# Kernel optimization log

Hardware: AMD Instinct MI355X
Metric: run time of the kernel (lower is better)

The kernel has to match this reference:

```python
import jax, jax.numpy as jnp
import numpy as np

B = 65536  # batch size

def setup_inputs() -> dict:
    key = jax.random.key(0)
    ks = jax.random.split(key, 6)
    x = jax.random.normal(ks[0], (B, 784), dtype=jnp.float32)
    conv_w = jax.random.normal(ks[1], (3, 3), dtype=jnp.float32) * 0.1
    in_size = (28 - 3 + 1) * (28 - 3 + 1)  # 676
    w1 = jax.random.normal(ks[2], (in_size, 300), dtype=jnp.float32) * 0.05
    b1 = jax.random.normal(ks[3], (300,), dtype=jnp.float32) * 0.05
    w2 = jax.random.normal(ks[4], (300, 10), dtype=jnp.float32) * 0.05
    b2 = jax.random.normal(ks[5], (10,), dtype=jnp.float32) * 0.05
    return {"x": x, "conv_w": conv_w, "w1": w1, "b1": b1, "w2": w2, "b2": b2}

def _convolve(img, conv_w):
    # img: [B,28,28]; conv_w: [kh,kw]. Valid cross-correlation (tensordot of each
    # window with the un-flipped kernel), matching the original Convolve().
    out = jax.lax.conv_general_dilated(
        img[:, None, :, :],            # [B,1,28,28]  NCHW
        conv_w[None, None, :, :],      # [1,1,3,3]    OIHW (no flip -> cross-correlation)
        window_strides=(1, 1),
        padding="VALID",
        dimension_numbers=("NCHW", "OIHW", "NCHW"),
    )
    return out[:, 0]  # [B,26,26]

def reference(x, conv_w, w1, b1, w2, b2):
    b = x.shape[0]
    img = x.reshape(b, 28, 28)
    feat = _convolve(img, conv_w).reshape(b, -1)      # [B,676]
    h1 = jax.nn.relu(feat @ w1 + b1)                  # [B,300]
    return h1 @ w2 + b2                               # [B,10]
```

## Files before the change

### kernel.cpp

```cpp
#include <hip/hip_runtime.h>
#include <hip/hip_bf16.h>

typedef __attribute__((ext_vector_type(8))) short bf16x8;
typedef __attribute__((ext_vector_type(4))) float f32x4;
typedef __attribute__((ext_vector_type(4))) unsigned int u32x4;
typedef unsigned short u16;
typedef unsigned int u32;

static constexpr int KDIM  = 784;
static constexpr int KP    = 800;
static constexpr int NDIM  = 300;
static constexpr int NP    = 320;
static constexpr int DDIM  = 10;
static constexpr int BM    = 256;
static constexpr int BK    = 32;
static constexpr int NSTEP = 25;
static constexpr int H1STR = 328;
static constexpr int NROW  = 65536;
static constexpr int NTHR  = 512;
static constexpr int ABYTES = 32768;
static constexpr int BBYTES = 20480;
static constexpr int BBASE  = 98304;

__device__ __forceinline__ u16 f2bf(float f) {
  unsigned u = __builtin_bit_cast(unsigned, f);
  u += 0x7fffu + ((u >> 16) & 1u);
  return (u16)(u >> 16);
}
__device__ __forceinline__ u32 pk2(float a, float b) {
  u32 r;
  asm("v_cvt_pk_bf16_f32 %0, %1, %2" : "=v"(r) : "v"(a), "v"(b));
  return r;
}
__device__ __forceinline__ void gll16(const void* g, void* l) {
  __builtin_amdgcn_global_load_lds(
      (const __attribute__((address_space(1))) void*)g,
      (__attribute__((address_space(3))) void*)l, 16, 0, 0);
}

__global__ void build_weff(const float* __restrict__ cw,
                           const float* __restrict__ w1,
                           u16* __restrict__ weff) {
  int idx = blockIdx.x * 256 + threadIdx.x;
  if (idx >= NP * KP) return;
  int n = idx / KP;
  int k = idx - n * KP;
  float acc = 0.f;
  if (n < NDIM && k < KDIM) {
    int r = k / 28, c = k - (k / 28) * 28;
    #pragma unroll
    for (int dr = 0; dr < 3; ++dr) {
      int orr = r - dr;
      if ((unsigned)orr < 26u) {
        #pragma unroll
        for (int dc = 0; dc < 3; ++dc) {
          int oc = c - dc;
          if ((unsigned)oc < 26u)
            acc += cw[dr * 3 + dc] * w1[(orr * 26 + oc) * NDIM + n];
        }
      }
    }
  }
  weff[n * KP + k] = f2bf(acc);
}

__global__ void __launch_bounds__(NTHR, 2)
fused_mlp(const float* __restrict__ x, const float* __restrict__ b1,
          const float* __restrict__ w2, const float* __restrict__ b2,
          const u16* __restrict__ weff, float* __restrict__ out) {
  __shared__ __align__(16) u16 lds[69632];

  const int tid  = threadIdx.x;
  const int wv   = tid >> 6;
  const int lane = tid & 63;
  const int l16  = lane & 15;
  const int lhi  = lane >> 4;
  const int wm   = wv >> 2;
  const int wn   = wv & 3;
  const int bm   = blockIdx.x * BM;
  const int wvn  = wn * 80;

  int aRow[4], aQg[4];
  #pragma unroll
  for (int it = 0; it < 4; ++it) {
    int s = tid + it * NTHR;
    aRow[it] = s >> 3;
    aQg[it]  = (s & 7) ^ (aRow[it] & 7);
  }
  int bRow[3], bQg[3];
  #pragma unroll
  for (int i = 0; i < 3; ++i) {
    int s = (i < 2) ? (tid + i * NTHR) : (1024 + (tid & 255));
    bRow[i] = s >> 2;
    bQg[i]  = (s & 3) ^ (bRow[i] & 3);
  }

  auto stageA = [&](int bufi, int t) {
    char* base = (char*)lds + bufi * ABYTES;
    int k0 = (t < NSTEP) ? t * BK : 0;
    #pragma unroll
    for (int it = 0; it < 4; ++it) {
      int kof = k0 + aQg[it] * 4;
      if (kof >= KDIM) kof = aQg[it] * 4;
      gll16(x + (size_t)(bm + aRow[it]) * KDIM + kof,
            base + (tid + it * NTHR) * 16);
    }
  };
  auto stageB = [&](int bufi, int t) {
    char* base = (char*)lds + BBASE + bufi * BBYTES;
    int k0 = (t < NSTEP) ? t * BK : 0;
    #pragma unroll
    for (int i = 0; i < 3; ++i) {
      int s = (i < 2) ? (tid + i * NTHR) : (1024 + (tid & 255));
      gll16(weff + (size_t)bRow[i] * KP + k0 + bQg[i] * 8, base + s * 16);
    }
  };

  f32x4 acc[8][5];
  #pragma unroll
  for (int mi = 0; mi < 8; ++mi)
    #pragma unroll
    for (int ni = 0; ni < 5; ++ni)
      acc[mi][ni] = (f32x4){0.f, 0.f, 0.f, 0.f};

  auto compute = [&](int abufi, int bbufi) {
    const f32x4* Af = (const f32x4*)((char*)lds + abufi * ABYTES);
    const u16*   Bb = (const u16*)((char*)lds + BBASE + bbufi * BBYTES);
    bf16x8 bfr[5];
    #pragma unroll
    for (int ni = 0; ni < 5; ++ni) {
      int n = wvn + ni * 16 + l16;
      int slot = n * 4 + (lhi ^ (n & 3));
      bfr[ni] = *reinterpret_cast<const bf16x8*>(Bb + slot * 8);
    }
    #pragma unroll
    for (int mi = 0; mi < 8; ++mi) {
      int R = wm * 128 + mi * 16 + l16;
      f32x4 a0 = Af[R * 8 + ((2 * lhi)     ^ (R & 7))];
      f32x4 a1 = Af[R * 8 + ((2 * lhi + 1) ^ (R & 7))];
      u32x4 amu = { pk2(a0[0], a0[1]), pk2(a0[2], a0[3]),
                    pk2(a1[0], a1[1]), pk2(a1[2], a1[3]) };
      bf16x8 am = __builtin_bit_cast(bf16x8, amu);
      #pragma unroll
      for (int ni = 0; ni < 5; ++ni)
        acc[mi][ni] = __builtin_amdgcn_mfma_f32_16x16x32_bf16(am, bfr[ni], acc[mi][ni], 0, 0, 0);
    }
  };

  stageA(0, 0);
  stageB(0, 0);
  stageA(1, 1);
  asm volatile("s_waitcnt vmcnt(4)" ::: "memory");
  __builtin_amdgcn_s_barrier();
  __builtin_amdgcn_sched_barrier(0);

  for (int t = 0; t < NSTEP; ++t) {
    stageB((t + 1) & 1, t + 1);
    stageA((t + 2) % 3, t + 2);
    __builtin_amdgcn_sched_barrier(0);
    compute(t % 3, t & 1);
    __builtin_amdgcn_sched_barrier(0);
    asm volatile("s_waitcnt vmcnt(4)" ::: "memory");
    __builtin_amdgcn_s_barrier();
    __builtin_amdgcn_sched_barrier(0);
  }
  __syncthreads();

  u16* H1  = lds;
  u16* W2T = lds + 20992;

  for (int i = tid; i < 16 * NP; i += NTHR) {
    int d = i / NP, n = i - (i / NP) * NP;
    float v = (d < DDIM && n < NDIM) ? w2[n * DDIM + d] : 0.f;
    W2T[d * H1STR + n] = f2bf(v);
  }
  float biasv[5];
  #pragma unroll
  for (int ni = 0; ni < 5; ++ni) {
    int col = wvn + ni * 16 + l16;
    biasv[ni] = (col < NDIM) ? b1[col] : 0.f;
  }

  #pragma unroll
  for (int p = 0; p < 4; ++p) {
    if (wm == (p >> 1)) {
      #pragma unroll
      for (int mj = 0; mj < 4; ++mj) {
        int mi = (p & 1) * 4 + mj;
        #pragma unroll
        for (int ni = 0; ni < 5; ++ni) {
          int col = wvn + ni * 16 + l16;
          int rb  = mj * 16 + lhi * 4;
          #pragma unroll
          for (int r = 0; r < 4; ++r) {
            float h = acc[mi][ni][r] + biasv[ni];
            H1[(rb + r) * H1STR + col] = f2bf(fmaxf(h, 0.f));
          }
        }
      }
    }
    __syncthreads();
    if (wv < 4) {
      f32x4 a2c = (f32x4){0.f, 0.f, 0.f, 0.f};
      #pragma unroll
      for (int ks = 0; ks < NP / 32; ++ks) {
        bf16x8 a2 = *reinterpret_cast<const bf16x8*>(
            H1 + (wv * 16 + l16) * H1STR + ks * 32 + lhi * 8);
        bf16x8 bw = *reinterpret_cast<const bf16x8*>(
            W2T + l16 * H1STR + ks * 32 + lhi * 8);
        a2c = __builtin_amdgcn_mfma_f32_16x16x32_bf16(a2, bw, a2c, 0, 0, 0);
      }
      if (l16 < DDIM) {
        float bb = b2[l16];
        #pragma unroll
        for (int r = 0; r < 4; ++r) {
          int row = bm + p * 64 + wv * 16 + lhi * 4 + r;
          out[(size_t)row * DDIM + l16] = a2c[r] + bb;
        }
      }
    }
    __syncthreads();
  }
}

extern "C" void kernel_launch(void* const* d_in, const int* in_sizes, int n_in,
                              void* d_out, int out_size, void* d_ws, size_t ws_size,
                              hipStream_t stream) {
  const float* x  = (const float*)d_in[0];
  const float* cw = (const float*)d_in[1];
  const float* w1 = (const float*)d_in[2];
  const float* b1 = (const float*)d_in[3];
  const float* w2 = (const float*)d_in[4];
  const float* b2 = (const float*)d_in[5];
  float* out = (float*)d_out;
  u16* weff = (u16*)d_ws;

  hipLaunchKernelGGL(build_weff, dim3((NP * KP + 255) / 256), dim3(256), 0, stream,
                     cw, w1, weff);
  hipLaunchKernelGGL(fused_mlp, dim3(NROW / BM), dim3(NTHR), 0, stream,
                     x, b1, w2, b2, weff, out);
}
```

Measured before the change: 61.70 us.

## Halve row tile to 128 and simplify to double-buffered pipeline

Shrinks the per-block row tile from 256 to 128, which halves the accumulator registers and the A staging buffers. LDS use drops from about 136KB to 72KB and the grid doubles to 512 blocks. The triple-buffered A pipeline with fine-grained vmcnt waits is replaced by simple double buffering with a full __syncthreads each step. The goal is better occupancy and load balance across CUs. In exchange, each B (weff) tile is reloaded by twice as many blocks, and the coarser sync gives less overlap of loads with compute.

```diff
diff --git a/kernel.cpp b/kernel.cpp
--- a/kernel.cpp
+++ b/kernel.cpp
@@ -12,15 +12,15 @@
 static constexpr int NDIM  = 300;
 static constexpr int NP    = 320;
 static constexpr int DDIM  = 10;
-static constexpr int BM    = 256;
+static constexpr int BM    = 128;
 static constexpr int BK    = 32;
 static constexpr int NSTEP = 25;
 static constexpr int H1STR = 328;
 static constexpr int NROW  = 65536;
 static constexpr int NTHR  = 512;
-static constexpr int ABYTES = 32768;
+static constexpr int ABYTES = 16384;
 static constexpr int BBYTES = 20480;
-static constexpr int BBASE  = 98304;
+static constexpr int BBASE  = 32768;
 
 __device__ __forceinline__ u16 f2bf(float f) {
   unsigned u = __builtin_bit_cast(unsigned, f);
@@ -68,7 +68,7 @@
 fused_mlp(const float* __restrict__ x, const float* __restrict__ b1,
           const float* __restrict__ w2, const float* __restrict__ b2,
           const u16* __restrict__ weff, float* __restrict__ out) {
-  __shared__ __align__(16) u16 lds[69632];
+  __shared__ __align__(16) u16 lds[36864];
 
   const int tid  = threadIdx.x;
   const int wv   = tid >> 6;
@@ -80,26 +80,27 @@
   const int bm   = blockIdx.x * BM;
   const int wvn  = wn * 80;
 
-  int aRow[4], aQg[4];
-  #pragma unroll
-  for (int it = 0; it < 4; ++it) {
+  int aRow[2], aQg[2];
+  #pragma unroll
+  for (int it = 0; it < 2; ++it) {
     int s = tid + it * NTHR;
     aRow[it] = s >> 3;
     aQg[it]  = (s & 7) ^ (aRow[it] & 7);
   }
-  int bRow[3], bQg[3];
+  int bRow[3], bQg[3], bSlot[3];
   #pragma unroll
   for (int i = 0; i < 3; ++i) {
     int s = (i < 2) ? (tid + i * NTHR) : (1024 + (tid & 255));
-    bRow[i] = s >> 2;
-    bQg[i]  = (s & 3) ^ (bRow[i] & 3);
+    bSlot[i] = s;
+    bRow[i]  = s >> 2;
+    bQg[i]   = (s & 3) ^ (bRow[i] & 3);
   }
 
   auto stageA = [&](int bufi, int t) {
     char* base = (char*)lds + bufi * ABYTES;
-    int k0 = (t < NSTEP) ? t * BK : 0;
-    #pragma unroll
-    for (int it = 0; it < 4; ++it) {
+    int k0 = t * BK;
+    #pragma unroll
+    for (int it = 0; it < 2; ++it) {
       int kof = k0 + aQg[it] * 4;
       if (kof >= KDIM) kof = aQg[it] * 4;
       gll16(x + (size_t)(bm + aRow[it]) * KDIM + kof,
@@ -108,24 +109,22 @@
   };
   auto stageB = [&](int bufi, int t) {
     char* base = (char*)lds + BBASE + bufi * BBYTES;
-    int k0 = (t < NSTEP) ? t * BK : 0;
-    #pragma unroll
-    for (int i = 0; i < 3; ++i) {
-      int s = (i < 2) ? (tid + i * NTHR) : (1024 + (tid & 255));
-      gll16(weff + (size_t)bRow[i] * KP + k0 + bQg[i] * 8, base + s * 16);
-    }
+    int k0 = t * BK;
+    #pragma unroll
+    for (int i = 0; i < 3; ++i)
+      gll16(weff + (size_t)bRow[i] * KP + k0 + bQg[i] * 8, base + bSlot[i] * 16);
   };
 
-  f32x4 acc[8][5];
-  #pragma unroll
-  for (int mi = 0; mi < 8; ++mi)
+  f32x4 acc[4][5];
+  #pragma unroll
+  for (int mi = 0; mi < 4; ++mi)
     #pragma unroll
     for (int ni = 0; ni < 5; ++ni)
       acc[mi][ni] = (f32x4){0.f, 0.f, 0.f, 0.f};
 
-  auto compute = [&](int abufi, int bbufi) {
-    const f32x4* Af = (const f32x4*)((char*)lds + abufi * ABYTES);
-    const u16*   Bb = (const u16*)((char*)lds + BBASE + bbufi * BBYTES);
+  auto compute = [&](int bufi) {
+    const f32x4* Af = (const f32x4*)((char*)lds + bufi * ABYTES);
+    const u16*   Bb = (const u16*)((char*)lds + BBASE + bufi * BBYTES);
     bf16x8 bfr[5];
     #pragma unroll
     for (int ni = 0; ni < 5; ++ni) {
@@ -134,8 +133,8 @@
       bfr[ni] = *reinterpret_cast<const bf16x8*>(Bb + slot * 8);
     }
     #pragma unroll
-    for (int mi = 0; mi < 8; ++mi) {
-      int R = wm * 128 + mi * 16 + l16;
+    for (int mi = 0; mi < 4; ++mi) {
+      int R = wm * 64 + mi * 16 + l16;
       f32x4 a0 = Af[R * 8 + ((2 * lhi)     ^ (R & 7))];
       f32x4 a1 = Af[R * 8 + ((2 * lhi + 1) ^ (R & 7))];
       u32x4 amu = { pk2(a0[0], a0[1]), pk2(a0[2], a0[3]),
@@ -149,22 +148,16 @@
 
   stageA(0, 0);
   stageB(0, 0);
-  stageA(1, 1);
-  asm volatile("s_waitcnt vmcnt(4)" ::: "memory");
-  __builtin_amdgcn_s_barrier();
-  __builtin_amdgcn_sched_barrier(0);
+  __syncthreads();
 
   for (int t = 0; t < NSTEP; ++t) {
-    stageB((t + 1) & 1, t + 1);
-    stageA((t + 2) % 3, t + 2);
-    __builtin_amdgcn_sched_barrier(0);
-    compute(t % 3, t & 1);
-    __builtin_amdgcn_sched_barrier(0);
-    asm volatile("s_waitcnt vmcnt(4)" ::: "memory");
-    __builtin_amdgcn_s_barrier();
-    __builtin_amdgcn_sched_barrier(0);
-  }
-  __syncthreads();
+    if (t + 1 < NSTEP) {
+      stageB((t + 1) & 1, t + 1);
+      stageA((t + 1) & 1, t + 1);
+    }
+    compute(t & 1);
+    __syncthreads();
+  }
 
   u16* H1  = lds;
   u16* W2T = lds + 20992;
@@ -182,15 +175,14 @@
   }
 
   #pragma unroll
-  for (int p = 0; p < 4; ++p) {
-    if (wm == (p >> 1)) {
+  for (int p = 0; p < 2; ++p) {
+    if (wm == p) {
       #pragma unroll
-      for (int mj = 0; mj < 4; ++mj) {
-        int mi = (p & 1) * 4 + mj;
+      for (int mi = 0; mi < 4; ++mi) {
         #pragma unroll
         for (int ni = 0; ni < 5; ++ni) {
           int col = wvn + ni * 16 + l16;
-          int rb  = mj * 16 + lhi * 4;
+          int rb  = mi * 16 + lhi * 4;
           #pragma unroll
           for (int r = 0; r < 4; ++r) {
             float h = acc[mi][ni][r] + biasv[ni];
```

Result: slower. 87.81 us (+42.3%).

## Load weight fragments directly from global and deepen A pipeline to four stages

Applied to the files above, without the earlier changes.

Drops LDS staging of the effective weight matrix and has each wave load its bf16 B fragments straight from global memory (L2-resident) into registers every K step. The freed LDS is used for a fourth x buffer, so the A prefetch runs three steps ahead. The goal is to remove B staging traffic and LDS reads, and to hide x load latency better. In exchange, the direct global B loads in the critical path add latency and redundant L2 traffic across waves. The vmcnt waits were changed to match the new per-thread load count.

```diff
diff --git a/kernel.cpp b/kernel.cpp
--- a/kernel.cpp
+++ b/kernel.cpp
@@ -19,8 +19,6 @@
 static constexpr int NROW  = 65536;
 static constexpr int NTHR  = 512;
 static constexpr int ABYTES = 32768;
-static constexpr int BBYTES = 20480;
-static constexpr int BBASE  = 98304;
 
 __device__ __forceinline__ u16 f2bf(float f) {
   unsigned u = __builtin_bit_cast(unsigned, f);
@@ -68,7 +66,7 @@
 fused_mlp(const float* __restrict__ x, const float* __restrict__ b1,
           const float* __restrict__ w2, const float* __restrict__ b2,
           const u16* __restrict__ weff, float* __restrict__ out) {
-  __shared__ __align__(16) u16 lds[69632];
+  __shared__ __align__(16) u16 lds[65536];
 
   const int tid  = threadIdx.x;
   const int wv   = tid >> 6;
@@ -87,13 +85,6 @@
     aRow[it] = s >> 3;
     aQg[it]  = (s & 7) ^ (aRow[it] & 7);
   }
-  int bRow[3], bQg[3];
-  #pragma unroll
-  for (int i = 0; i < 3; ++i) {
-    int s = (i < 2) ? (tid + i * NTHR) : (1024 + (tid & 255));
-    bRow[i] = s >> 2;
-    bQg[i]  = (s & 3) ^ (bRow[i] & 3);
-  }
 
   auto stageA = [&](int bufi, int t) {
     char* base = (char*)lds + bufi * ABYTES;
@@ -106,15 +97,11 @@
             base + (tid + it * NTHR) * 16);
     }
   };
-  auto stageB = [&](int bufi, int t) {
-    char* base = (char*)lds + BBASE + bufi * BBYTES;
-    int k0 = (t < NSTEP) ? t * BK : 0;
-    #pragma unroll
-    for (int i = 0; i < 3; ++i) {
-      int s = (i < 2) ? (tid + i * NTHR) : (1024 + (tid & 255));
-      gll16(weff + (size_t)bRow[i] * KP + k0 + bQg[i] * 8, base + s * 16);
-    }
-  };
+
+  int bOff[5];
+  #pragma unroll
+  for (int ni = 0; ni < 5; ++ni)
+    bOff[ni] = (wvn + ni * 16 + l16) * KP + lhi * 8;
 
   f32x4 acc[8][5];
   #pragma unroll
@@ -123,16 +110,23 @@
     for (int ni = 0; ni < 5; ++ni)
       acc[mi][ni] = (f32x4){0.f, 0.f, 0.f, 0.f};
 
-  auto compute = [&](int abufi, int bbufi) {
-    const f32x4* Af = (const f32x4*)((char*)lds + abufi * ABYTES);
-    const u16*   Bb = (const u16*)((char*)lds + BBASE + bbufi * BBYTES);
+  stageA(0, 0);
+  stageA(1, 1);
+  stageA(2, 2);
+  asm volatile("s_waitcnt vmcnt(8)" ::: "memory");
+  __builtin_amdgcn_s_barrier();
+  __builtin_amdgcn_sched_barrier(0);
+
+  for (int t = 0; t < NSTEP; ++t) {
     bf16x8 bfr[5];
     #pragma unroll
-    for (int ni = 0; ni < 5; ++ni) {
-      int n = wvn + ni * 16 + l16;
-      int slot = n * 4 + (lhi ^ (n & 3));
-      bfr[ni] = *reinterpret_cast<const bf16x8*>(Bb + slot * 8);
-    }
+    for (int ni = 0; ni < 5; ++ni)
+      bfr[ni] = *reinterpret_cast<const bf16x8*>(weff + bOff[ni] + t * BK);
+    __builtin_amdgcn_sched_barrier(0);
+    stageA((t + 3) & 3, t + 3);
+    __builtin_amdgcn_sched_barrier(0);
+
+    const f32x4* Af = (const f32x4*)((char*)lds + (t & 3) * ABYTES);
     #pragma unroll
     for (int mi = 0; mi < 8; ++mi) {
       int R = wm * 128 + mi * 16 + l16;
@@ -145,20 +139,6 @@
       for (int ni = 0; ni < 5; ++ni)
         acc[mi][ni] = __builtin_amdgcn_mfma_f32_16x16x32_bf16(am, bfr[ni], acc[mi][ni], 0, 0, 0);
     }
-  };
-
-  stageA(0, 0);
-  stageB(0, 0);
-  stageA(1, 1);
-  asm volatile("s_waitcnt vmcnt(4)" ::: "memory");
-  __builtin_amdgcn_s_barrier();
-  __builtin_amdgcn_sched_barrier(0);
-
-  for (int t = 0; t < NSTEP; ++t) {
-    stageB((t + 1) & 1, t + 1);
-    stageA((t + 2) % 3, t + 2);
-    __builtin_amdgcn_sched_barrier(0);
-    compute(t % 3, t & 1);
     __builtin_amdgcn_sched_barrier(0);
     asm volatile("s_waitcnt vmcnt(4)" ::: "memory");
     __builtin_amdgcn_s_barrier();
```

New measurement: 77.64 us. 1.26x slower.

## Stage w1 rows in LDS for weff build and halve epilogue passes

Applied to the files above, without the earlier changes.

Rewrites build_weff to run one block per input image row. Each block stages the three contributing w1 rows in shared memory, computes the folded weights, and writes them out through an LDS transpose so the global stores are coalesced instead of strided reads from global memory. The fused kernel's epilogue now stores 128 rows of H1 per pass and uses all 8 waves for the second GEMM, so it runs 2 passes instead of 4 and needs fewer barriers. The trade-off is that build_weff launches only 28 blocks, which leaves most CUs idle and adds some LDS reindexing work.

```diff
diff --git a/kernel.cpp b/kernel.cpp
--- a/kernel.cpp
+++ b/kernel.cpp
@@ -19,8 +19,8 @@
 static constexpr int NROW  = 65536;
 static constexpr int NTHR  = 512;
 static constexpr int ABYTES = 32768;
-static constexpr int BBYTES = 20480;
-static constexpr int BBASE  = 98304;
+static constexpr int BBASEU = 49152;
+static constexpr int BU     = 10240;
 
 __device__ __forceinline__ u16 f2bf(float f) {
   unsigned u = __builtin_bit_cast(unsigned, f);
@@ -38,30 +38,56 @@
       (__attribute__((address_space(3))) void*)l, 16, 0, 0);
 }
 
-__global__ void build_weff(const float* __restrict__ cw,
-                           const float* __restrict__ w1,
-                           u16* __restrict__ weff) {
-  int idx = blockIdx.x * 256 + threadIdx.x;
-  if (idx >= NP * KP) return;
-  int n = idx / KP;
-  int k = idx - n * KP;
-  float acc = 0.f;
-  if (n < NDIM && k < KDIM) {
-    int r = k / 28, c = k - (k / 28) * 28;
-    #pragma unroll
-    for (int dr = 0; dr < 3; ++dr) {
-      int orr = r - dr;
-      if ((unsigned)orr < 26u) {
-        #pragma unroll
-        for (int dc = 0; dc < 3; ++dc) {
-          int oc = c - dc;
-          if ((unsigned)oc < 26u)
-            acc += cw[dr * 3 + dc] * w1[(orr * 26 + oc) * NDIM + n];
+__global__ void __launch_bounds__(256)
+build_weff(const float* __restrict__ cw, const float* __restrict__ w1,
+           u16* __restrict__ weff) {
+  __shared__ float w1s[78 * 300];
+  __shared__ u16 outT[NP * 28];
+
+  const int r   = blockIdx.x;
+  const int tid = threadIdx.x;
+
+  for (int i = tid; i < 3 * 7800; i += 256) {
+    int j = i / 7800, rem = i - j * 7800;
+    int orr = r - 2 + j;
+    w1s[i] = ((unsigned)orr < 26u) ? w1[orr * 7800 + rem] : 0.f;
+  }
+  float c9[9];
+  #pragma unroll
+  for (int q = 0; q < 9; ++q) c9[q] = cw[q];
+  __syncthreads();
+
+  for (int i = tid; i < NP * 28; i += 256) {
+    int n = i / 28, c = i - (i / 28) * 28;
+    float acc = 0.f;
+    if (n < NDIM) {
+      #pragma unroll
+      for (int dr = 0; dr < 3; ++dr) {
+        int orr = r - dr;
+        if ((unsigned)orr < 26u) {
+          #pragma unroll
+          for (int dc = 0; dc < 3; ++dc) {
+            int oc = c - dc;
+            if ((unsigned)oc < 26u)
+              acc += c9[dr * 3 + dc] * w1s[((2 - dr) * 26 + oc) * 300 + n];
+          }
         }
       }
     }
-  }
-  weff[n * KP + k] = f2bf(acc);
+    outT[i] = f2bf(acc);
+  }
+  __syncthreads();
+
+  for (int i = tid; i < NP * 28; i += 256) {
+    int n = i / 28, c = i - (i / 28) * 28;
+    weff[n * KP + r * 28 + c] = outT[i];
+  }
+  if (r == 27) {
+    for (int i = tid; i < NP * 16; i += 256) {
+      int n = i / 16, kk = 784 + (i - (i / 16) * 16);
+      weff[n * KP + kk] = (u16)0;
+    }
+  }
 }
 
 __global__ void __launch_bounds__(NTHR, 2)
@@ -87,12 +113,13 @@
     aRow[it] = s >> 3;
     aQg[it]  = (s & 7) ^ (aRow[it] & 7);
   }
-  int bRow[3], bQg[3];
+  int bRow[3], bQg[3], bSlot[3];
   #pragma unroll
   for (int i = 0; i < 3; ++i) {
     int s = (i < 2) ? (tid + i * NTHR) : (1024 + (tid & 255));
-    bRow[i] = s >> 2;
-    bQg[i]  = (s & 3) ^ (bRow[i] & 3);
+    bSlot[i] = s;
+    bRow[i]  = s >> 2;
+    bQg[i]   = (s & 3) ^ (bRow[i] & 3);
   }
 
   auto stageA = [&](int bufi, int t) {
@@ -107,13 +134,11 @@
     }
   };
   auto stageB = [&](int bufi, int t) {
-    char* base = (char*)lds + BBASE + bufi * BBYTES;
+    char* base = (char*)(lds + BBASEU + bufi * BU);
     int k0 = (t < NSTEP) ? t * BK : 0;
     #pragma unroll
-    for (int i = 0; i < 3; ++i) {
-      int s = (i < 2) ? (tid + i * NTHR) : (1024 + (tid & 255));
-      gll16(weff + (size_t)bRow[i] * KP + k0 + bQg[i] * 8, base + s * 16);
-    }
+    for (int i = 0; i < 3; ++i)
+      gll16(weff + (size_t)bRow[i] * KP + k0 + bQg[i] * 8, base + bSlot[i] * 16);
   };
 
   f32x4 acc[8][5];
@@ -125,7 +150,7 @@
 
   auto compute = [&](int abufi, int bbufi) {
     const f32x4* Af = (const f32x4*)((char*)lds + abufi * ABYTES);
-    const u16*   Bb = (const u16*)((char*)lds + BBASE + bbufi * BBYTES);
+    const u16*   Bb = lds + BBASEU + bbufi * BU;
     bf16x8 bfr[5];
     #pragma unroll
     for (int ni = 0; ni < 5; ++ni) {
@@ -167,7 +192,7 @@
   __syncthreads();
 
   u16* H1  = lds;
-  u16* W2T = lds + 20992;
+  u16* W2T = lds + 128 * H1STR;
 
   for (int i = tid; i < 16 * NP; i += NTHR) {
     int d = i / NP, n = i - (i / NP) * NP;
@@ -182,15 +207,14 @@
   }
 
   #pragma unroll
-  for (int p = 0; p < 4; ++p) {
-    if (wm == (p >> 1)) {
-      #pragma unroll
-      for (int mj = 0; mj < 4; ++mj) {
-        int mi = (p & 1) * 4 + mj;
+  for (int p = 0; p < 2; ++p) {
+    if (wm == p) {
+      #pragma unroll
+      for (int mi = 0; mi < 8; ++mi) {
         #pragma unroll
         for (int ni = 0; ni < 5; ++ni) {
           int col = wvn + ni * 16 + l16;
-          int rb  = mj * 16 + lhi * 4;
+          int rb  = mi * 16 + lhi * 4;
           #pragma unroll
           for (int r = 0; r < 4; ++r) {
             float h = acc[mi][ni][r] + biasv[ni];
@@ -200,7 +224,7 @@
       }
     }
     __syncthreads();
-    if (wv < 4) {
+    {
       f32x4 a2c = (f32x4){0.f, 0.f, 0.f, 0.f};
       #pragma unroll
       for (int ks = 0; ks < NP / 32; ++ks) {
@@ -214,7 +238,7 @@
         float bb = b2[l16];
         #pragma unroll
         for (int r = 0; r < 4; ++r) {
-          int row = bm + p * 64 + wv * 16 + lhi * 4 + r;
+          int row = bm + p * 128 + wv * 16 + lhi * 4 + r;
           out[(size_t)row * DDIM + l16] = a2c[r] + bb;
         }
       }
@@ -235,8 +259,7 @@
   float* out = (float*)d_out;
   u16* weff = (u16*)d_ws;
 
-  hipLaunchKernelGGL(build_weff, dim3((NP * KP + 255) / 256), dim3(256), 0, stream,
-                     cw, w1, weff);
+  hipLaunchKernelGGL(build_weff, dim3(28), dim3(256), 0, stream, cw, w1, weff);
   hipLaunchKernelGGL(fused_mlp, dim3(NROW / BM), dim3(NTHR), 0, stream,
                      x, b1, w2, b2, weff, out);
 }
```

Measured after the change: 99.62 us. 1.61x slower.
